# Performance work log

Measured on AMD Instinct MI355X. Metric: run time of the kernel, lower is better.

Reference implementation:

```python
import jax, jax.numpy as jnp
import numpy as np

HIDDEN = 3072
INTER = 8192
B, S = 4, 2048


def setup_inputs() -> dict:
    key = jax.random.key(0)
    k1, k2, k3, k4, k5 = jax.random.split(key, 5)
    hidden_states = jax.random.normal(k1, (B, S, HIDDEN), dtype=jnp.float32)
    # int8-valued quantized weights (stored as int32), per-output-channel scales
    gate_up_w_q = jax.random.randint(k2, (2 * INTER, HIDDEN), -128, 128, dtype=jnp.int32)
    gate_up_scale = jax.random.uniform(k3, (2 * INTER,), dtype=jnp.float32) * 0.01
    down_w_q = jax.random.randint(k4, (HIDDEN, INTER), -128, 128, dtype=jnp.int32)
    down_scale = jax.random.uniform(k5, (HIDDEN,), dtype=jnp.float32) * 0.01
    return {
        "hidden_states": hidden_states,
        "gate_up_w_q": gate_up_w_q,
        "gate_up_scale": gate_up_scale,
        "down_w_q": down_w_q,
        "down_scale": down_scale,
    }


def reference(hidden_states, gate_up_w_q, gate_up_scale, down_w_q, down_scale):
    # Inline dequant: W = W_q * scale (per output channel)
    w_gu = gate_up_w_q.astype(jnp.float32) * gate_up_scale[:, None]   # [2I, H]
    up_states = jnp.einsum("bsh,oh->bso", hidden_states, w_gu)        # [B, S, 2I]
    gate, up = jnp.split(up_states, 2, axis=-1)                       # each [B, S, I]
    h = up * jax.nn.silu(gate)                                        # SwiGLU
    w_d = down_w_q.astype(jnp.float32) * down_scale[:, None]          # [H, I]
    return jnp.einsum("bsi,hi->bsh", h, w_d)                          # [B, S, H]
```

## Files before the change

### kernel.cpp

```cpp
#include <hip/hip_runtime.h>
#include <hip/hip_bf16.h>

#define HIDDEN 3072
#define INTER  8192
#define NTOK   8192

typedef __attribute__((ext_vector_type(8))) short bf16x8;
typedef __attribute__((ext_vector_type(4))) float f32x4;

__device__ __forceinline__ void gload_lds16(const void* g, void* l) {
  __builtin_amdgcn_global_load_lds(
      (const __attribute__((address_space(1))) void*)g,
      (__attribute__((address_space(3))) void*)l, 16, 0, 0);
}

__device__ __forceinline__ unsigned short f2bf(float f) {
  unsigned int u = __builtin_bit_cast(unsigned int, f);
  u += 0x7fffu + ((u >> 16) & 1u);
  return (unsigned short)(u >> 16);
}


__global__ void cvt_f32_bf16(const float* __restrict__ in,
                             unsigned short* __restrict__ out, int n4) {
  int i = blockIdx.x * blockDim.x + threadIdx.x;
  if (i >= n4) return;
  float4 v = reinterpret_cast<const float4*>(in)[i];
  ushort4 o;
  o.x = f2bf(v.x); o.y = f2bf(v.y); o.z = f2bf(v.z); o.w = f2bf(v.w);
  reinterpret_cast<ushort4*>(out)[i] = o;
}

__global__ void cvt_i32_bf16(const int* __restrict__ in,
                             unsigned short* __restrict__ out, int n4) {
  int i = blockIdx.x * blockDim.x + threadIdx.x;
  if (i >= n4) return;
  int4 v = reinterpret_cast<const int4*>(in)[i];
  ushort4 o;
  o.x = f2bf((float)v.x); o.y = f2bf((float)v.y);
  o.z = f2bf((float)v.z); o.w = f2bf((float)v.w);
  reinterpret_cast<ushort4*>(out)[i] = o;
}

__global__ void cvt_wgu_perm(const int* __restrict__ in,
                             unsigned short* __restrict__ out) {
  int i4 = blockIdx.x * blockDim.x + threadIdx.x;
  const int RW = HIDDEN / 4;
  if (i4 >= 2 * INTER * RW) return;
  int rowp = i4 / RW;
  int col4 = i4 - rowp * RW;
  int c = ((rowp >> 5) << 4) + (rowp & 15);
  int u = (rowp >> 4) & 1;
  int srow = u * INTER + c;
  int4 v = reinterpret_cast<const int4*>(in)[(size_t)srow * RW + col4];
  ushort4 o;
  o.x = f2bf((float)v.x); o.y = f2bf((float)v.y);
  o.z = f2bf((float)v.z); o.w = f2bf((float)v.w);
  reinterpret_cast<ushort4*>(out)[i4] = o;
}


template<int K, int N, int MODE>
__global__ __launch_bounds__(512, 2) void gemm8p(
    const unsigned short* __restrict__ A,
    const unsigned short* __restrict__ B,
    const float* __restrict__ scale,
    void* __restrict__ outv)
{
  constexpr int NT = K / 64;
  __shared__ __align__(16) unsigned short lds[2][2][2][256 * 32];

  const int nbn = N / 256;
  const int nwg = (NTOK / 256) * nbn;
  int bid = blockIdx.x;
  int wg = (bid & 7) * (nwg >> 3) + (bid >> 3);
  const int bm = (wg / nbn) * 256;
  const int bn = (wg % nbn) * 256;

  const int tid  = threadIdx.x;
  const int lane = tid & 63;
  const int wid  = tid >> 6;
  const int wr = wid >> 2;
  const int wc = wid & 3;

  const int srow0 = tid >> 2;
  const int srow1 = 128 + (tid >> 2);
  const int scb   = tid & 3;

  const unsigned short* Ab = A + (size_t)bm * K;
  const unsigned short* Bb = B + (size_t)bn * K;

  auto stage = [&](const unsigned short* Gb, int op, int tt, int kh) {
    if (tt >= NT) return;
    int p = tt & 1;
    int kc = tt * 64 + kh * 32;
    unsigned short* lbase = &lds[p][op][kh][0];
    gload_lds16(Gb + (size_t)srow0 * K + kc + ((scb ^ ((srow0 >> 1) & 3)) * 8),
                lbase + (size_t)tid * 8);
    gload_lds16(Gb + (size_t)srow1 * K + kc + ((scb ^ ((srow1 >> 1) & 3)) * 8),
                lbase + (size_t)(512 + tid) * 8);
  };

  auto readA = [&](int p, int kh, int m) -> bf16x8 {
    int row = wr * 128 + m * 16 + (lane & 15);
    int cb = (lane >> 4) ^ ((row >> 1) & 3);
    return *(const bf16x8*)&lds[p][0][kh][row * 32 + cb * 8];
  };
  auto readB = [&](int p, int kh, int n) -> bf16x8 {
    int row = wc * 64 + n * 16 + (lane & 15);
    int cb = (lane >> 4) ^ ((row >> 1) & 3);
    return *(const bf16x8*)&lds[p][1][kh][row * 32 + cb * 8];
  };

  f32x4 acc[8][4] = {};
  bf16x8 aP[4], aQ[4], bP[4], bQ[4];

  stage(Ab, 0, 0, 0);
  stage(Bb, 1, 0, 0);
  stage(Ab, 0, 0, 1);
  stage(Bb, 1, 0, 1);
  asm volatile("s_waitcnt vmcnt(4)" ::: "memory");
  __builtin_amdgcn_s_barrier();
#pragma unroll
  for (int m = 0; m < 4; ++m) aP[m] = readA(0, 0, m);
#pragma unroll
  for (int n = 0; n < 4; ++n) bP[n] = readB(0, 0, n);

  for (int t = 0; t < NT; ++t) {
    const int pr = t & 1;

#pragma unroll
    for (int m = 0; m < 4; ++m) aQ[m] = readA(pr, 0, m + 4);
    stage(Ab, 0, t + 1, 0);
    __builtin_amdgcn_s_setprio(1);
#pragma unroll
    for (int m = 0; m < 4; ++m)
#pragma unroll
      for (int n = 0; n < 4; ++n)
        acc[m][n] = __builtin_amdgcn_mfma_f32_16x16x32_bf16(aP[m], bP[n], acc[m][n], 0, 0, 0);
    __builtin_amdgcn_s_setprio(0);

    if (t + 1 < NT) {
      asm volatile("s_waitcnt vmcnt(2)" ::: "memory");
    } else {
      asm volatile("s_waitcnt vmcnt(0)" ::: "memory");
    }
    __builtin_amdgcn_s_barrier();
#pragma unroll
    for (int m = 0; m < 4; ++m) aP[m] = readA(pr, 1, m);
#pragma unroll
    for (int n = 0; n < 4; ++n) bQ[n] = readB(pr, 1, n);
    stage(Bb, 1, t + 1, 0);
    __builtin_amdgcn_s_setprio(1);
#pragma unroll
    for (int m = 0; m < 4; ++m)
#pragma unroll
      for (int n = 0; n < 4; ++n)
        acc[m + 4][n] = __builtin_amdgcn_mfma_f32_16x16x32_bf16(aQ[m], bP[n], acc[m + 4][n], 0, 0, 0);
    __builtin_amdgcn_s_setprio(0);

#pragma unroll
    for (int m = 0; m < 4; ++m) aQ[m] = readA(pr, 1, m + 4);
    stage(Ab, 0, t + 1, 1);
    __builtin_amdgcn_s_setprio(1);
#pragma unroll
    for (int m = 0; m < 4; ++m)
#pragma unroll
      for (int n = 0; n < 4; ++n)
        acc[m][n] = __builtin_amdgcn_mfma_f32_16x16x32_bf16(aP[m], bQ[n], acc[m][n], 0, 0, 0);
    __builtin_amdgcn_s_setprio(0);

    asm volatile("s_waitcnt vmcnt(2)" ::: "memory");
    __builtin_amdgcn_s_barrier();
    if (t + 1 < NT) {
#pragma unroll
      for (int m = 0; m < 4; ++m) aP[m] = readA(pr ^ 1, 0, m);
#pragma unroll
      for (int n = 0; n < 4; ++n) bP[n] = readB(pr ^ 1, 0, n);
    }
    stage(Bb, 1, t + 1, 1);
    __builtin_amdgcn_s_setprio(1);
#pragma unroll
    for (int m = 0; m < 4; ++m)
#pragma unroll
      for (int n = 0; n < 4; ++n)
        acc[m + 4][n] = __builtin_amdgcn_mfma_f32_16x16x32_bf16(aQ[m], bQ[n], acc[m + 4][n], 0, 0, 0);
    __builtin_amdgcn_s_setprio(0);
  }

  const int crow0 = (lane >> 4) * 4;
  const int ccol  = lane & 15;
  if constexpr (MODE == 1) {
    unsigned short* H = (unsigned short*)outv;
    const int hbase = (bn >> 1) + wc * 32;
#pragma unroll
    for (int np = 0; np < 2; ++np) {
      int hcol = hbase + np * 16 + ccol;
      float sg = scale[hcol];
      float su = scale[INTER + hcol];
#pragma unroll
      for (int m = 0; m < 8; ++m) {
#pragma unroll
        for (int j = 0; j < 4; ++j) {
          int row = bm + wr * 128 + m * 16 + crow0 + j;
          float g = acc[m][2 * np + 0][j] * sg;
          float u = acc[m][2 * np + 1][j] * su;
          float s = g / (1.0f + __expf(-g));
          H[(size_t)row * INTER + hcol] = f2bf(u * s);
        }
      }
    }
  } else {
    float* O = (float*)outv;
#pragma unroll
    for (int n = 0; n < 4; ++n) {
      int col = bn + wc * 64 + n * 16 + ccol;
      float sc = scale[col];
#pragma unroll
      for (int m = 0; m < 8; ++m) {
#pragma unroll
        for (int j = 0; j < 4; ++j) {
          int row = bm + wr * 128 + m * 16 + crow0 + j;
          O[(size_t)row * N + col] = acc[m][n][j] * sc;
        }
      }
    }
  }
}


extern "C" void kernel_launch(void* const* d_in, const int* in_sizes, int n_in,
                              void* d_out, int out_size, void* d_ws, size_t ws_size,
                              hipStream_t stream) {
  (void)in_sizes; (void)n_in; (void)out_size; (void)ws_size;

  const float* hidden = (const float*)d_in[0];
  const int*   guq    = (const int*)d_in[1];
  const float* gus    = (const float*)d_in[2];
  const int*   dwq    = (const int*)d_in[3];
  const float* dsc    = (const float*)d_in[4];
  float* out = (float*)d_out;

  char* ws = (char*)d_ws;
  unsigned short* xb  = (unsigned short*)(ws);
  unsigned short* wgu = (unsigned short*)(ws + 50331648ull);
  unsigned short* wd  = (unsigned short*)(ws + 150994944ull);
  unsigned short* hb  = (unsigned short*)(ws + 201326592ull);

  {
    int n4 = NTOK * HIDDEN / 4;
    cvt_f32_bf16<<<(n4 + 255) / 256, 256, 0, stream>>>(hidden, xb, n4);
  }
  {
    int n4 = 2 * INTER * HIDDEN / 4;
    cvt_wgu_perm<<<(n4 + 255) / 256, 256, 0, stream>>>(guq, wgu);
  }
  {
    int n4 = HIDDEN * INTER / 4;
    cvt_i32_bf16<<<(n4 + 255) / 256, 256, 0, stream>>>(dwq, wd, n4);
  }

  gemm8p<HIDDEN, 2 * INTER, 1>
      <<<(NTOK / 256) * (2 * INTER / 256), 512, 0, stream>>>(xb, wgu, gus, hb);
  gemm8p<INTER, HIDDEN, 2>
      <<<(NTOK / 256) * (HIDDEN / 256), 512, 0, stream>>>(hb, wd, dsc, out);
}
```

Before: 1.241 ms.

## Use dedicated 128x256 tile kernel for down projection GEMM

```diff
diff --git a/kernel.cpp b/kernel.cpp
--- a/kernel.cpp
+++ b/kernel.cpp
@@ -60,12 +60,12 @@
 }
 
 
-template<int K, int N, int MODE>
+template<int K, int N>
 __global__ __launch_bounds__(512, 2) void gemm8p(
     const unsigned short* __restrict__ A,
     const unsigned short* __restrict__ B,
     const float* __restrict__ scale,
-    void* __restrict__ outv)
+    unsigned short* __restrict__ H)
 {
   constexpr int NT = K / 64;
   __shared__ __align__(16) unsigned short lds[2][2][2][256 * 32];
@@ -126,6 +126,7 @@
 #pragma unroll
   for (int n = 0; n < 4; ++n) bP[n] = readB(0, 0, n);
 
+#pragma unroll 2
   for (int t = 0; t < NT; ++t) {
     const int pr = t & 1;
 
@@ -190,39 +191,152 @@
 
   const int crow0 = (lane >> 4) * 4;
   const int ccol  = lane & 15;
-  if constexpr (MODE == 1) {
-    unsigned short* H = (unsigned short*)outv;
-    const int hbase = (bn >> 1) + wc * 32;
-#pragma unroll
-    for (int np = 0; np < 2; ++np) {
-      int hcol = hbase + np * 16 + ccol;
-      float sg = scale[hcol];
-      float su = scale[INTER + hcol];
-#pragma unroll
-      for (int m = 0; m < 8; ++m) {
-#pragma unroll
-        for (int j = 0; j < 4; ++j) {
-          int row = bm + wr * 128 + m * 16 + crow0 + j;
-          float g = acc[m][2 * np + 0][j] * sg;
-          float u = acc[m][2 * np + 1][j] * su;
-          float s = g / (1.0f + __expf(-g));
-          H[(size_t)row * INTER + hcol] = f2bf(u * s);
-        }
+  const int hbase = (bn >> 1) + wc * 32;
+#pragma unroll
+  for (int np = 0; np < 2; ++np) {
+    int hcol = hbase + np * 16 + ccol;
+    float sg = scale[hcol];
+    float su = scale[INTER + hcol];
+#pragma unroll
+    for (int m = 0; m < 8; ++m) {
+#pragma unroll
+      for (int j = 0; j < 4; ++j) {
+        int row = bm + wr * 128 + m * 16 + crow0 + j;
+        float g = acc[m][2 * np + 0][j] * sg;
+        float u = acc[m][2 * np + 1][j] * su;
+        float s = g / (1.0f + __expf(-g));
+        H[(size_t)row * INTER + hcol] = f2bf(u * s);
       }
     }
-  } else {
-    float* O = (float*)outv;
-#pragma unroll
-    for (int n = 0; n < 4; ++n) {
-      int col = bn + wc * 64 + n * 16 + ccol;
-      float sc = scale[col];
-#pragma unroll
-      for (int m = 0; m < 8; ++m) {
-#pragma unroll
-        for (int j = 0; j < 4; ++j) {
-          int row = bm + wr * 128 + m * 16 + crow0 + j;
-          O[(size_t)row * N + col] = acc[m][n][j] * sc;
-        }
+  }
+}
+
+
+__global__ __launch_bounds__(512, 2) void gemm2k(
+    const unsigned short* __restrict__ A,
+    const unsigned short* __restrict__ B,
+    const float* __restrict__ scale,
+    float* __restrict__ O)
+{
+  constexpr int K = INTER;
+  constexpr int NT = K / 64;
+  __shared__ __align__(16) unsigned short ldsA[2][2][128 * 32];
+  __shared__ __align__(16) unsigned short ldsB[2][2][256 * 32];
+
+  const int nbn = HIDDEN / 256;
+  const int nwg = (NTOK / 128) * nbn;
+  int bid = blockIdx.x;
+  int wg = (bid & 7) * (nwg >> 3) + (bid >> 3);
+  const int bm = (wg / nbn) * 128;
+  const int bn = (wg % nbn) * 256;
+
+  const int tid  = threadIdx.x;
+  const int lane = tid & 63;
+  const int wid  = tid >> 6;
+  const int wr = wid >> 2;
+  const int wc = wid & 3;
+
+  const int srow0 = tid >> 2;
+  const int srow1 = 128 + (tid >> 2);
+  const int scb   = tid & 3;
+
+  const unsigned short* Ab = A + (size_t)bm * K;
+  const unsigned short* Bb = B + (size_t)bn * K;
+
+  auto stageA = [&](int tt, int kh) {
+    if (tt >= NT) return;
+    int p = tt & 1;
+    int kc = tt * 64 + kh * 32;
+    gload_lds16(Ab + (size_t)srow0 * K + kc + ((scb ^ ((srow0 >> 1) & 3)) * 8),
+                &ldsA[p][kh][0] + (size_t)tid * 8);
+  };
+  auto stageB = [&](int tt, int kh) {
+    if (tt >= NT) return;
+    int p = tt & 1;
+    int kc = tt * 64 + kh * 32;
+    unsigned short* lbase = &ldsB[p][kh][0];
+    gload_lds16(Bb + (size_t)srow0 * K + kc + ((scb ^ ((srow0 >> 1) & 3)) * 8),
+                lbase + (size_t)tid * 8);
+    gload_lds16(Bb + (size_t)srow1 * K + kc + ((scb ^ ((srow1 >> 1) & 3)) * 8),
+                lbase + (size_t)(512 + tid) * 8);
+  };
+
+  auto readA = [&](int p, int kh, int m) -> bf16x8 {
+    int row = wr * 64 + m * 16 + (lane & 15);
+    int cb = (lane >> 4) ^ ((row >> 1) & 3);
+    return *(const bf16x8*)&ldsA[p][kh][row * 32 + cb * 8];
+  };
+  auto readB = [&](int p, int kh, int n) -> bf16x8 {
+    int row = wc * 64 + n * 16 + (lane & 15);
+    int cb = (lane >> 4) ^ ((row >> 1) & 3);
+    return *(const bf16x8*)&ldsB[p][kh][row * 32 + cb * 8];
+  };
+
+  f32x4 acc[4][4] = {};
+  bf16x8 aF[4], bF[4];
+
+  stageA(0, 0);
+  stageB(0, 0);
+  stageA(0, 1);
+  stageB(0, 1);
+  asm volatile("s_waitcnt vmcnt(3)" ::: "memory");
+  __builtin_amdgcn_s_barrier();
+
+#pragma unroll 2
+  for (int t = 0; t < NT; ++t) {
+    const int pr = t & 1;
+
+#pragma unroll
+    for (int m = 0; m < 4; ++m) aF[m] = readA(pr, 0, m);
+#pragma unroll
+    for (int n = 0; n < 4; ++n) bF[n] = readB(pr, 0, n);
+    stageA(t + 1, 0);
+    __builtin_amdgcn_s_setprio(1);
+#pragma unroll
+    for (int m = 0; m < 4; ++m)
+#pragma unroll
+      for (int n = 0; n < 4; ++n)
+        acc[m][n] = __builtin_amdgcn_mfma_f32_16x16x32_bf16(aF[m], bF[n], acc[m][n], 0, 0, 0);
+    __builtin_amdgcn_s_setprio(0);
+
+    stageB(t + 1, 0);
+    if (t + 1 < NT) {
+      asm volatile("s_waitcnt vmcnt(3)" ::: "memory");
+    } else {
+      asm volatile("s_waitcnt vmcnt(0)" ::: "memory");
+    }
+    __builtin_amdgcn_s_barrier();
+
+#pragma unroll
+    for (int m = 0; m < 4; ++m) aF[m] = readA(pr, 1, m);
+#pragma unroll
+    for (int n = 0; n < 4; ++n) bF[n] = readB(pr, 1, n);
+    stageA(t + 1, 1);
+    __builtin_amdgcn_s_setprio(1);
+#pragma unroll
+    for (int m = 0; m < 4; ++m)
+#pragma unroll
+      for (int n = 0; n < 4; ++n)
+        acc[m][n] = __builtin_amdgcn_mfma_f32_16x16x32_bf16(aF[m], bF[n], acc[m][n], 0, 0, 0);
+    __builtin_amdgcn_s_setprio(0);
+
+    stageB(t + 1, 1);
+    asm volatile("s_waitcnt vmcnt(3)" ::: "memory");
+    __builtin_amdgcn_s_barrier();
+  }
+
+  const int crow0 = (lane >> 4) * 4;
+  const int ccol  = lane & 15;
+#pragma unroll
+  for (int n = 0; n < 4; ++n) {
+    int col = bn + wc * 64 + n * 16 + ccol;
+    float sc = scale[col];
+#pragma unroll
+    for (int m = 0; m < 4; ++m) {
+#pragma unroll
+      for (int j = 0; j < 4; ++j) {
+        int row = bm + wr * 64 + m * 16 + crow0 + j;
+        O[(size_t)row * HIDDEN + col] = acc[m][n][j] * sc;
       }
     }
   }
@@ -260,8 +374,7 @@
     cvt_i32_bf16<<<(n4 + 255) / 256, 256, 0, stream>>>(dwq, wd, n4);
   }
 
-  gemm8p<HIDDEN, 2 * INTER, 1>
+  gemm8p<HIDDEN, 2 * INTER>
       <<<(NTOK / 256) * (2 * INTER / 256), 512, 0, stream>>>(xb, wgu, gus, hb);
-  gemm8p<INTER, HIDDEN, 2>
-      <<<(NTOK / 256) * (HIDDEN / 256), 512, 0, stream>>>(hb, wd, dsc, out);
-}
+  gemm2k<<<(NTOK / 128) * (HIDDEN / 256), 512, 0, stream>>>(hb, wd, dsc, out);
+}
```

Result: slower. 2.710 ms (+118.4%).

## Use 128x256 single-stage gate/up GEMM and 192-wide tiles for down GEMM

Applied to the files above, without the earlier changes.

```diff
diff --git a/kernel.cpp b/kernel.cpp
--- a/kernel.cpp
+++ b/kernel.cpp
@@ -60,22 +60,139 @@
 }
 
 
-template<int K, int N, int MODE>
-__global__ __launch_bounds__(512, 2) void gemm8p(
+__global__ __launch_bounds__(256, 2) void gemm1_2blk(
     const unsigned short* __restrict__ A,
     const unsigned short* __restrict__ B,
     const float* __restrict__ scale,
-    void* __restrict__ outv)
+    unsigned short* __restrict__ H)
 {
+  constexpr int K = HIDDEN;
+  constexpr int N = 2 * INTER;
+  constexpr int NT = K / 32;
+  __shared__ __align__(16) unsigned short ldsA[2][128 * 32];
+  __shared__ __align__(16) unsigned short ldsB[2][256 * 32];
+
+  const int nbn = N / 256;
+  const int nwg = (NTOK / 128) * nbn;
+  int bid = blockIdx.x;
+  int wg = (bid & 7) * (nwg >> 3) + (bid >> 3);
+  const int bm = (wg / nbn) * 128;
+  const int bn = (wg % nbn) * 256;
+
+  const int tid  = threadIdx.x;
+  const int lane = tid & 63;
+  const int wc   = tid >> 6;
+
+  const int srow = tid >> 2;
+  const int scb  = tid & 3;
+
+  const unsigned short* Ab = A + (size_t)bm * K;
+  const unsigned short* Bb = B + (size_t)bn * K;
+
+  auto stageA = [&](int tt) {
+    if (tt >= NT) return;
+    int p = tt & 1;
+    int kc = tt * 32;
+#pragma unroll
+    for (int inst = 0; inst < 2; ++inst) {
+      int row = inst * 64 + srow;
+      gload_lds16(Ab + (size_t)row * K + kc + ((scb ^ ((row >> 1) & 3)) * 8),
+                  &ldsA[p][(size_t)(inst * 256 + tid) * 8]);
+    }
+  };
+  auto stageB = [&](int tt) {
+    if (tt >= NT) return;
+    int p = tt & 1;
+    int kc = tt * 32;
+#pragma unroll
+    for (int inst = 0; inst < 4; ++inst) {
+      int row = inst * 64 + srow;
+      gload_lds16(Bb + (size_t)row * K + kc + ((scb ^ ((row >> 1) & 3)) * 8),
+                  &ldsB[p][(size_t)(inst * 256 + tid) * 8]);
+    }
+  };
+
+  auto readA = [&](int p, int m) -> bf16x8 {
+    int row = m * 16 + (lane & 15);
+    int cb = (lane >> 4) ^ ((row >> 1) & 3);
+    return *(const bf16x8*)&ldsA[p][row * 32 + cb * 8];
+  };
+  auto readB = [&](int p, int n) -> bf16x8 {
+    int row = wc * 64 + n * 16 + (lane & 15);
+    int cb = (lane >> 4) ^ ((row >> 1) & 3);
+    return *(const bf16x8*)&ldsB[p][row * 32 + cb * 8];
+  };
+
+  f32x4 acc[8][4] = {};
+  bf16x8 aF[8], bF[4];
+
+  stageA(0);
+  stageB(0);
+  asm volatile("s_waitcnt vmcnt(0)" ::: "memory");
+  __builtin_amdgcn_s_barrier();
+
+  for (int t = 0; t < NT; ++t) {
+    const int pr = t & 1;
+
+    stageA(t + 1);
+    stageB(t + 1);
+
+#pragma unroll
+    for (int m = 0; m < 8; ++m) aF[m] = readA(pr, m);
+#pragma unroll
+    for (int n = 0; n < 4; ++n) bF[n] = readB(pr, n);
+
+    __builtin_amdgcn_s_setprio(1);
+#pragma unroll
+    for (int m = 0; m < 8; ++m)
+#pragma unroll
+      for (int n = 0; n < 4; ++n)
+        acc[m][n] = __builtin_amdgcn_mfma_f32_16x16x32_bf16(aF[m], bF[n], acc[m][n], 0, 0, 0);
+    __builtin_amdgcn_s_setprio(0);
+
+    asm volatile("s_waitcnt vmcnt(0)" ::: "memory");
+    __builtin_amdgcn_s_barrier();
+  }
+
+  const int crow0 = (lane >> 4) * 4;
+  const int ccol  = lane & 15;
+  const int hbase = (bn >> 1) + wc * 32;
+#pragma unroll
+  for (int np = 0; np < 2; ++np) {
+    int hcol = hbase + np * 16 + ccol;
+    float sg = scale[hcol];
+    float su = scale[INTER + hcol];
+#pragma unroll
+    for (int m = 0; m < 8; ++m) {
+#pragma unroll
+      for (int j = 0; j < 4; ++j) {
+        int row = bm + m * 16 + crow0 + j;
+        float g = acc[m][2 * np + 0][j] * sg;
+        float u = acc[m][2 * np + 1][j] * su;
+        float s = g / (1.0f + __expf(-g));
+        H[(size_t)row * INTER + hcol] = f2bf(u * s);
+      }
+    }
+  }
+}
+
+
+__global__ __launch_bounds__(512, 2) void gemm2_192(
+    const unsigned short* __restrict__ A,
+    const unsigned short* __restrict__ B,
+    const float* __restrict__ scale,
+    float* __restrict__ O)
+{
+  constexpr int K = INTER;
   constexpr int NT = K / 64;
   __shared__ __align__(16) unsigned short lds[2][2][2][256 * 32];
 
-  const int nbn = N / 256;
+  const int nbn = HIDDEN / 192;
   const int nwg = (NTOK / 256) * nbn;
   int bid = blockIdx.x;
   int wg = (bid & 7) * (nwg >> 3) + (bid >> 3);
   const int bm = (wg / nbn) * 256;
-  const int bn = (wg % nbn) * 256;
+  const int bn = (wg % nbn) * 192;
 
   const int tid  = threadIdx.x;
   const int lane = tid & 63;
@@ -107,13 +224,13 @@
     return *(const bf16x8*)&lds[p][0][kh][row * 32 + cb * 8];
   };
   auto readB = [&](int p, int kh, int n) -> bf16x8 {
-    int row = wc * 64 + n * 16 + (lane & 15);
+    int row = wc * 48 + n * 16 + (lane & 15);
     int cb = (lane >> 4) ^ ((row >> 1) & 3);
     return *(const bf16x8*)&lds[p][1][kh][row * 32 + cb * 8];
   };
 
-  f32x4 acc[8][4] = {};
-  bf16x8 aP[4], aQ[4], bP[4], bQ[4];
+  f32x4 acc[8][3] = {};
+  bf16x8 aP[4], aQ[4], bP[3], bQ[3];
 
   stage(Ab, 0, 0, 0);
   stage(Bb, 1, 0, 0);
@@ -124,7 +241,7 @@
 #pragma unroll
   for (int m = 0; m < 4; ++m) aP[m] = readA(0, 0, m);
 #pragma unroll
-  for (int n = 0; n < 4; ++n) bP[n] = readB(0, 0, n);
+  for (int n = 0; n < 3; ++n) bP[n] = readB(0, 0, n);
 
   for (int t = 0; t < NT; ++t) {
     const int pr = t & 1;
@@ -136,7 +253,7 @@
 #pragma unroll
     for (int m = 0; m < 4; ++m)
 #pragma unroll
-      for (int n = 0; n < 4; ++n)
+      for (int n = 0; n < 3; ++n)
         acc[m][n] = __builtin_amdgcn_mfma_f32_16x16x32_bf16(aP[m], bP[n], acc[m][n], 0, 0, 0);
     __builtin_amdgcn_s_setprio(0);
 
@@ -149,13 +266,13 @@
 #pragma unroll
     for (int m = 0; m < 4; ++m) aP[m] = readA(pr, 1, m);
 #pragma unroll
-    for (int n = 0; n < 4; ++n) bQ[n] = readB(pr, 1, n);
+    for (int n = 0; n < 3; ++n) bQ[n] = readB(pr, 1, n);
     stage(Bb, 1, t + 1, 0);
     __builtin_amdgcn_s_setprio(1);
 #pragma unroll
     for (int m = 0; m < 4; ++m)
 #pragma unroll
-      for (int n = 0; n < 4; ++n)
+      for (int n = 0; n < 3; ++n)
         acc[m + 4][n] = __builtin_amdgcn_mfma_f32_16x16x32_bf16(aQ[m], bP[n], acc[m + 4][n], 0, 0, 0);
     __builtin_amdgcn_s_setprio(0);
 
@@ -166,7 +283,7 @@
 #pragma unroll
     for (int m = 0; m < 4; ++m)
 #pragma unroll
-      for (int n = 0; n < 4; ++n)
+      for (int n = 0; n < 3; ++n)
         acc[m][n] = __builtin_amdgcn_mfma_f32_16x16x32_bf16(aP[m], bQ[n], acc[m][n], 0, 0, 0);
     __builtin_amdgcn_s_setprio(0);
 
@@ -176,53 +293,30 @@
 #pragma unroll
       for (int m = 0; m < 4; ++m) aP[m] = readA(pr ^ 1, 0, m);
 #pragma unroll
-      for (int n = 0; n < 4; ++n) bP[n] = readB(pr ^ 1, 0, n);
+      for (int n = 0; n < 3; ++n) bP[n] = readB(pr ^ 1, 0, n);
     }
     stage(Bb, 1, t + 1, 1);
     __builtin_amdgcn_s_setprio(1);
 #pragma unroll
     for (int m = 0; m < 4; ++m)
 #pragma unroll
-      for (int n = 0; n < 4; ++n)
+      for (int n = 0; n < 3; ++n)
         acc[m + 4][n] = __builtin_amdgcn_mfma_f32_16x16x32_bf16(aQ[m], bQ[n], acc[m + 4][n], 0, 0, 0);
     __builtin_amdgcn_s_setprio(0);
   }
 
   const int crow0 = (lane >> 4) * 4;
   const int ccol  = lane & 15;
-  if constexpr (MODE == 1) {
-    unsigned short* H = (unsigned short*)outv;
-    const int hbase = (bn >> 1) + wc * 32;
-#pragma unroll
-    for (int np = 0; np < 2; ++np) {
-      int hcol = hbase + np * 16 + ccol;
-      float sg = scale[hcol];
-      float su = scale[INTER + hcol];
-#pragma unroll
-      for (int m = 0; m < 8; ++m) {
-#pragma unroll
-        for (int j = 0; j < 4; ++j) {
-          int row = bm + wr * 128 + m * 16 + crow0 + j;
-          float g = acc[m][2 * np + 0][j] * sg;
-          float u = acc[m][2 * np + 1][j] * su;
-          float s = g / (1.0f + __expf(-g));
-          H[(size_t)row * INTER + hcol] = f2bf(u * s);
-        }
-      }
-    }
-  } else {
-    float* O = (float*)outv;
-#pragma unroll
-    for (int n = 0; n < 4; ++n) {
-      int col = bn + wc * 64 + n * 16 + ccol;
-      float sc = scale[col];
-#pragma unroll
-      for (int m = 0; m < 8; ++m) {
-#pragma unroll
-        for (int j = 0; j < 4; ++j) {
-          int row = bm + wr * 128 + m * 16 + crow0 + j;
-          O[(size_t)row * N + col] = acc[m][n][j] * sc;
-        }
+#pragma unroll
+  for (int n = 0; n < 3; ++n) {
+    int col = bn + wc * 48 + n * 16 + ccol;
+    float sc = scale[col];
+#pragma unroll
+    for (int m = 0; m < 8; ++m) {
+#pragma unroll
+      for (int j = 0; j < 4; ++j) {
+        int row = bm + wr * 128 + m * 16 + crow0 + j;
+        O[(size_t)row * HIDDEN + col] = acc[m][n][j] * sc;
       }
     }
   }
@@ -260,8 +354,6 @@
     cvt_i32_bf16<<<(n4 + 255) / 256, 256, 0, stream>>>(dwq, wd, n4);
   }
 
-  gemm8p<HIDDEN, 2 * INTER, 1>
-      <<<(NTOK / 256) * (2 * INTER / 256), 512, 0, stream>>>(xb, wgu, gus, hb);
-  gemm8p<INTER, HIDDEN, 2>
-      <<<(NTOK / 256) * (HIDDEN / 256), 512, 0, stream>>>(hb, wd, dsc, out);
-}
+  gemm1_2blk<<<(NTOK / 128) * (2 * INTER / 256), 256, 0, stream>>>(xb, wgu, gus, hb);
+  gemm2_192<<<(NTOK / 256) * (HIDDEN / 192), 512, 0, stream>>>(hb, wd, dsc, out);
+}
```

Result: slower. 1.520 ms (+22.4%).
